# Optimization experiments

Measured on AMD Instinct MI355X. Metric: run time of the kernel, lower is better.

The kernel has to match this reference:

```python
import jax, jax.numpy as jnp
import numpy as np

N, IN_CH, HID, OUT = 3072, 128, 256, 32
HEADS = 12


def setup_inputs() -> dict:
    key = jax.random.key(0)
    ks = jax.random.split(key, 16)

    def glorot(k, shape):
        fan_in, fan_out = shape[0], shape[-1]
        lim = float(np.sqrt(6.0 / (fan_in + fan_out)))
        return jax.random.uniform(k, shape, jnp.float32, -lim, lim)

    return {
        "x": jax.random.normal(ks[0], (N, IN_CH), jnp.float32),
        "attn_tensor": jax.random.normal(ks[1], (HEADS, N, N), jnp.float32),
        "edge_weight": jnp.ones((1,), jnp.float32),  # unused (use_edge_weight=False)
        "batch_idx": jnp.zeros((N,), jnp.int64),      # single graph
        # Conv2d(12,1,1) == per-head scalar mix
        "agg_w": jax.random.normal(ks[2], (HEADS,), jnp.float32) * 0.1,
        "agg_b": jnp.zeros((1,), jnp.float32),
        # GCNConv weights (x @ W then propagate, + bias)
        "W1": glorot(ks[3], (IN_CH, HID)), "b1": jnp.zeros((HID,), jnp.float32),
        "W2": glorot(ks[4], (HID, HID)),   "b2": jnp.zeros((HID,), jnp.float32),
        # final MLP: Linear -> ReLU -> LayerNorm -> Linear
        "lin1_W": glorot(ks[5], (HID, HID)), "lin1_b": jnp.zeros((HID,), jnp.float32),
        "ln_g": jnp.ones((HID,), jnp.float32), "ln_b": jnp.zeros((HID,), jnp.float32),
        "lin2_W": glorot(ks[6], (HID, OUT)), "lin2_b": jnp.zeros((OUT,), jnp.float32),
    }


def reference(x, attn_tensor, edge_weight, batch_idx,
              agg_w, agg_b, W1, b1, W2, b2,
              lin1_W, lin1_b, ln_g, ln_b, lin2_W, lin2_b):
    threshold = 0.0
    n = x.shape[0]

    # Conv2d(12,1,kernel_size=1): weighted sum over heads -> [N, N] score matrix
    agg = jnp.einsum('c,cij->ij', agg_w, attn_tensor) + agg_b[0]

    # thresholded adjacency (mask.nonzero() -> edge_index), kept dense in jax
    A = (agg > threshold).astype(x.dtype)  # A[s, t] = edge s->t

    # PyG gcn_norm with add_remaining_self_loops (binary weights -> diag = 1)
    eye = jnp.eye(n, dtype=x.dtype)
    A_hat = A * (1.0 - eye) + eye
    deg = A_hat.sum(axis=0)                        # in-degree at target nodes
    dinv = jnp.where(deg > 0, jax.lax.rsqrt(deg), 0.0)
    A_norm = dinv[:, None] * A_hat * dinv[None, :]  # norm = dinv[src] * dinv[dst]

    # GCNConv 1: out[t] = sum_s A_norm[s,t] (x W)[s] + b
    h = jnp.einsum('st,sd->td', A_norm, x @ W1) + b1
    h = jax.nn.relu(h)
    # GCNConv 2
    h = jnp.einsum('st,sd->td', A_norm, h @ W2) + b2

    # global_mean_pool over batch_idx (single graph here)
    bi = batch_idx.astype(jnp.int32)
    sums = jax.ops.segment_sum(h, bi, num_segments=1)
    counts = jax.ops.segment_sum(jnp.ones((n,), h.dtype), bi, num_segments=1)
    g = sums / counts[:, None]

    # Linear -> ReLU -> LayerNorm -> Linear
    z = jax.nn.relu(g @ lin1_W + lin1_b)
    mu = z.mean(axis=-1, keepdims=True)
    var = ((z - mu) ** 2).mean(axis=-1, keepdims=True)
    z = (z - mu) * jax.lax.rsqrt(var + 1e-5) * ln_g + ln_b
    out = z @ lin2_W + lin2_b
    return out
```

## Files before the change

kernel.cpp:

```cpp
#include <hip/hip_runtime.h>
#include <hip/hip_bf16.h>

#define NN     3072
#define NW32   96
#define INCH   128
#define HID    256
#define NHEADS 12
#define PLANE  9437184LL

typedef __attribute__((ext_vector_type(8))) short     s16x8;
typedef __attribute__((ext_vector_type(4))) float     f32x4;
typedef __attribute__((ext_vector_type(8))) unsigned short u16x8;
typedef __attribute__((ext_vector_type(4))) unsigned int   u32x4;

__device__ inline unsigned short bf16_rne(float f) {
    unsigned int u = __float_as_uint(f);
    u += 0x7FFFu + ((u >> 16) & 1u);
    return (unsigned short)(u >> 16);
}

__global__ __launch_bounds__(256) void k_adj_y1(const float* __restrict__ attn,
                                                const float* __restrict__ agg_w,
                                                const float* __restrict__ agg_b,
                                                const float* __restrict__ x,
                                                const float* __restrict__ W1,
                                                unsigned int* __restrict__ maskT32,
                                                unsigned short* __restrict__ y1t) {
    __shared__ unsigned int chunkU[4][64];
    __shared__ float xs[8][INCH];

    if (blockIdx.x < 1152) {
        const int w = threadIdx.x >> 6, l = threadIdx.x & 63;
        const int t0 = (blockIdx.x % 12) * 256;
        const int s0 = (blockIdx.x / 12) * 32;
        const int tb = t0 + 4 * l;

        float wc[NHEADS];
#pragma unroll
        for (int c = 0; c < NHEADS; ++c) wc[c] = agg_w[c];
        const float bias = agg_b[0];

        const float* base = attn + (long long)(s0 + 8 * w) * NN + tb;
        unsigned int colb = 0;
#pragma unroll 2
        for (int i = 0; i < 8; ++i) {
            const int s = s0 + 8 * w + i;
            const float* ps = base + (long long)i * NN;
            f32x4 acc = {bias, bias, bias, bias};
#pragma unroll
            for (int c = 0; c < NHEADS; ++c) {
                f32x4 v = *(const f32x4*)(ps + c * PLANE);
                acc[0] = fmaf(wc[c], v[0], acc[0]);
                acc[1] = fmaf(wc[c], v[1], acc[1]);
                acc[2] = fmaf(wc[c], v[2], acc[2]);
                acc[3] = fmaf(wc[c], v[3], acc[3]);
            }
            unsigned int bset = 0;
            bset |= (acc[0] > 0.0f || s == tb + 0) ? (1u << i)        : 0u;
            bset |= (acc[1] > 0.0f || s == tb + 1) ? (1u << (8 + i))  : 0u;
            bset |= (acc[2] > 0.0f || s == tb + 2) ? (1u << (16 + i)) : 0u;
            bset |= (acc[3] > 0.0f || s == tb + 3) ? (1u << (24 + i)) : 0u;
            colb |= bset;
        }
        chunkU[w][l] = colb;
        __syncthreads();
        const int l2 = threadIdx.x >> 2, j = threadIdx.x & 3;
        unsigned int word =  ((chunkU[0][l2] >> (8 * j)) & 0xFFu)
                          | (((chunkU[1][l2] >> (8 * j)) & 0xFFu) << 8)
                          | (((chunkU[2][l2] >> (8 * j)) & 0xFFu) << 16)
                          | (((chunkU[3][l2] >> (8 * j)) & 0xFFu) << 24);
        maskT32[(long long)(t0 + threadIdx.x) * NW32 + (s0 >> 5)] = word;
    } else {
        int s0 = (blockIdx.x - 1152) * 8;
        for (int i = threadIdx.x; i < 8 * INCH; i += 256)
            xs[i >> 7][i & 127] = x[s0 * INCH + i];
        __syncthreads();
        int d = threadIdx.x;
        float acc[8] = {0, 0, 0, 0, 0, 0, 0, 0};
        for (int k = 0; k < INCH; ++k) {
            float w = W1[k * HID + d];
#pragma unroll
            for (int r = 0; r < 8; ++r) acc[r] = fmaf(xs[r][k], w, acc[r]);
        }
        u16x8 v;
#pragma unroll
        for (int r = 0; r < 8; ++r) v[r] = bf16_rne(acc[r]);
        *(u16x8*)(y1t + (long long)d * NN + s0) = v;
    }
}

__global__ __launch_bounds__(256) void k_dinv(const unsigned int* __restrict__ maskT32,
                                              float* __restrict__ dinv,
                                              unsigned short* __restrict__ dinvb) {
    int t = blockIdx.x * 256 + threadIdx.x;
    const u32x4* row = (const u32x4*)(maskT32 + (long long)t * NW32);
    int deg = 0;
#pragma unroll
    for (int i = 0; i < 24; ++i) {
        u32x4 v = row[i];
        deg += __popc(v[0]) + __popc(v[1]) + __popc(v[2]) + __popc(v[3]);
    }
    float di = rsqrtf((float)deg);
    dinv[t] = di;
    dinvb[t] = bf16_rne(di);
}

__global__ __launch_bounds__(256) void k_prop(const unsigned int* __restrict__ maskT32,
                                              const unsigned short* __restrict__ dinvb,
                                              const unsigned short* __restrict__ y1t,
                                              const float* __restrict__ dinv,
                                              float* __restrict__ partials,
                                              float* __restrict__ w2p) {
    if (blockIdx.x < 384) {
        const int w = threadIdx.x >> 6, l = threadIdx.x & 63;
        const int lr = l & 15, lg = l >> 4;
        const int t0 = (blockIdx.x % 48) * 64 + w * 16;
        const int d0 = ((blockIdx.x / 48) % 2) * 128;
        const int z  = blockIdx.x / 96;

        const unsigned long long* mrow =
            (const unsigned long long*)(maskT32 + (long long)(t0 + lr) * NW32) + z * 12;

        const unsigned short* B[8];
#pragma unroll
        for (int n = 0; n < 8; ++n)
            B[n] = y1t + (long long)(d0 + n * 16 + lr) * NN;

        f32x4 acc[8];
#pragma unroll
        for (int n = 0; n < 8; ++n) acc[n] = (f32x4){0.f, 0.f, 0.f, 0.f};

#pragma unroll 2
        for (int kw = 0; kw < 12; ++kw) {
            unsigned long long word = mrow[kw];
#pragma unroll
            for (int half = 0; half < 2; ++half) {
                const int k0 = z * 768 + kw * 64 + half * 32 + lg * 8;
                unsigned int bits = (unsigned int)((word >> (half * 32 + lg * 8)) & 0xFFULL);
                u16x8 dv = *(const u16x8*)(dinvb + k0);
                s16x8 av;
#pragma unroll
                for (int j = 0; j < 8; ++j)
                    av[j] = ((bits >> j) & 1u) ? (short)dv[j] : (short)0;
#pragma unroll
                for (int n = 0; n < 8; ++n) {
                    s16x8 bv = *(const s16x8*)(const void*)(B[n] + k0);
                    acc[n] = __builtin_amdgcn_mfma_f32_16x16x32_bf16(av, bv, acc[n], 0, 0, 0);
                }
            }
        }

        const int trow = t0 + lg * 4;
#pragma unroll
        for (int n = 0; n < 8; ++n) {
            const int d = d0 + n * 16 + lr;
#pragma unroll
            for (int r = 0; r < 4; ++r)
                partials[((size_t)z * NN + trow + r) * HID + d] = acc[n][r];
        }
    } else {
        __shared__ float red[4][64];
        const int r = blockIdx.x - 384;
        const int wq = r % 48;
        const int tc = r / 48;
        const int wv = threadIdx.x >> 6, l = threadIdx.x & 63;
        const unsigned long long* mt = (const unsigned long long*)maskT32;
        float acc = 0.0f;
#pragma unroll 4
        for (int it = 0; it < 64; ++it) {
            const int t = tc * 256 + wv * 64 + it;
            unsigned long long word = mt[(long long)t * 48 + wq];
            acc += ((word >> l) & 1ULL) ? dinv[t] : 0.0f;
        }
        red[wv][l] = acc;
        __syncthreads();
        if (threadIdx.x < 64)
            w2p[tc * NN + wq * 64 + threadIdx.x] =
                red[0][threadIdx.x] + red[1][threadIdx.x] + red[2][threadIdx.x] + red[3][threadIdx.x];
    }
}

__global__ __launch_bounds__(256) void k_vred(const float* __restrict__ partials,
                                              const float* __restrict__ dinv,
                                              const float* __restrict__ b1,
                                              const float* __restrict__ w2p,
                                              float* __restrict__ vp) {
    __shared__ float w2s[8];
    const int b = blockIdx.x, d = threadIdx.x;
    if (threadIdx.x < 8) {
        const int t = b * 8 + threadIdx.x;
        float a = 0.0f;
#pragma unroll
        for (int tc = 0; tc < 12; ++tc) a += w2p[tc * NN + t];
        w2s[threadIdx.x] = dinv[t] * a;
    }
    __syncthreads();
    const float bb = b1[d];
    float vacc = 0.0f;
#pragma unroll
    for (int i = 0; i < 8; ++i) {
        const int t = b * 8 + i;
        float ssum = partials[((size_t)0 * NN + t) * HID + d]
                   + partials[((size_t)1 * NN + t) * HID + d]
                   + partials[((size_t)2 * NN + t) * HID + d]
                   + partials[((size_t)3 * NN + t) * HID + d];
        float h = fmaxf(fmaf(dinv[t], ssum, bb), 0.0f);
        vacc = fmaf(w2s[i], h, vacc);
    }
    vp[b * HID + d] = vacc;
}

__global__ __launch_bounds__(256) void k_head(const float* __restrict__ vp,
                                              const float* __restrict__ W2,
                                              const float* __restrict__ b2,
                                              const float* __restrict__ l1W,
                                              const float* __restrict__ l1b,
                                              const float* __restrict__ lng,
                                              const float* __restrict__ lnb,
                                              const float* __restrict__ l2W,
                                              const float* __restrict__ l2b,
                                              float* __restrict__ out) {
    __shared__ float vs[HID], gs[HID], zs[HID], red[4];
    int d = threadIdx.x;
    float v = 0.0f;
    for (int c = 0; c < 384; ++c) v += vp[c * HID + d];
    vs[d] = v;
    __syncthreads();
    float a = 0.0f;
    for (int k = 0; k < HID; ++k) a = fmaf(vs[k], W2[k * HID + d], a);
    gs[d] = b2[d] + a * (1.0f / 3072.0f);
    __syncthreads();
    float z1 = l1b[d];
    for (int k = 0; k < HID; ++k) z1 = fmaf(gs[k], l1W[k * HID + d], z1);
    z1 = fmaxf(z1, 0.0f);
    float sum = z1;
    for (int o = 1; o < 64; o <<= 1) sum += __shfl_xor(sum, o);
    if ((d & 63) == 0) red[d >> 6] = sum;
    __syncthreads();
    float mu = (red[0] + red[1] + red[2] + red[3]) * (1.0f / 256.0f);
    __syncthreads();
    float diff = z1 - mu, sq = diff * diff;
    for (int o = 1; o < 64; o <<= 1) sq += __shfl_xor(sq, o);
    if ((d & 63) == 0) red[d >> 6] = sq;
    __syncthreads();
    float var = (red[0] + red[1] + red[2] + red[3]) * (1.0f / 256.0f);
    float zn = diff * rsqrtf(var + 1e-5f) * lng[d] + lnb[d];
    zs[d] = zn;
    __syncthreads();
    if (d < 32) {
        float o = l2b[d];
        for (int k = 0; k < HID; ++k) o = fmaf(zs[k], l2W[k * 32 + d], o);
        out[d] = o;
    }
}

extern "C" void kernel_launch(void* const* d_in, const int* in_sizes, int n_in,
                              void* d_out, int out_size, void* d_ws, size_t ws_size,
                              hipStream_t stream) {
    const float* x     = (const float*)d_in[0];
    const float* attn  = (const float*)d_in[1];
    const float* agg_w = (const float*)d_in[4];
    const float* agg_b = (const float*)d_in[5];
    const float* W1    = (const float*)d_in[6];
    const float* b1    = (const float*)d_in[7];
    const float* W2    = (const float*)d_in[8];
    const float* b2    = (const float*)d_in[9];
    const float* l1W   = (const float*)d_in[10];
    const float* l1b   = (const float*)d_in[11];
    const float* lng   = (const float*)d_in[12];
    const float* lnb   = (const float*)d_in[13];
    const float* l2W   = (const float*)d_in[14];
    const float* l2b   = (const float*)d_in[15];
    float* out = (float*)d_out;

    char* ws = (char*)d_ws;
    size_t off = 0;
    auto alloc = [&](size_t bytes) -> void* {
        off = (off + 255) & ~(size_t)255;
        void* p = ws + off;
        off += bytes;
        return p;
    };
    unsigned int*   maskT32 = (unsigned int*)alloc((size_t)NN * NW32 * 4);
    float*          dinv  = (float*)alloc((size_t)NN * 4);
    unsigned short* dinvb = (unsigned short*)alloc((size_t)NN * 2);
    float*          w2p   = (float*)alloc((size_t)12 * NN * 4);
    unsigned short* y1t   = (unsigned short*)alloc((size_t)HID * NN * 2);
    float*          part  = (float*)alloc((size_t)4 * NN * HID * 4);
    float*          vp    = (float*)alloc((size_t)384 * HID * 4);

    hipLaunchKernelGGL(k_adj_y1, dim3(1536), dim3(256), 0, stream,
                       attn, agg_w, agg_b, x, W1, maskT32, y1t);
    hipLaunchKernelGGL(k_dinv,   dim3(12),   dim3(256), 0, stream, maskT32, dinv, dinvb);
    hipLaunchKernelGGL(k_prop,   dim3(960),  dim3(256), 0, stream,
                       maskT32, dinvb, y1t, dinv, part, w2p);
    hipLaunchKernelGGL(k_vred,   dim3(384),  dim3(256), 0, stream, part, dinv, b1, w2p, vp);
    hipLaunchKernelGGL(k_head,   dim3(1),    dim3(256), 0, stream,
                       vp, W2, b2, l1W, l1b, lng, lnb, l2W, l2b, out);
}
```

Baseline: 191.7 us.

## Reorder head-mix loads with nontemporal hints and fuse final head via last-block counter

The adjacency kernel now loops over heads outermost, keeping eight row accumulators in registers and issuing nontemporal loads over the large attention tensor. The bias becomes a negated threshold in the comparison. The separate single-block head kernel is folded into the reduction kernel: a global atomic counter, reset in the degree kernel, lets the last finishing block run the MLP head, removing one launch. This adds threadfence and atomic overhead and more register pressure in the adjacency kernel.

```diff
diff --git a/kernel.cpp b/kernel.cpp
--- a/kernel.cpp
+++ b/kernel.cpp
@@ -34,33 +34,36 @@
         const int t0 = (blockIdx.x % 12) * 256;
         const int s0 = (blockIdx.x / 12) * 32;
         const int tb = t0 + 4 * l;
-
-        float wc[NHEADS];
-#pragma unroll
-        for (int c = 0; c < NHEADS; ++c) wc[c] = agg_w[c];
-        const float bias = agg_b[0];
-
-        const float* base = attn + (long long)(s0 + 8 * w) * NN + tb;
+        const int srow = s0 + 8 * w;
+        const float thr = -agg_b[0];
+
+        f32x4 acc[8];
+#pragma unroll
+        for (int i = 0; i < 8; ++i) acc[i] = (f32x4){0.f, 0.f, 0.f, 0.f};
+
+        const int voff = srow * NN + tb;
+#pragma unroll 1
+        for (int c = 0; c < NHEADS; ++c) {
+            const float* pc = attn + (long long)c * PLANE;
+            const float wcv = agg_w[c];
+#pragma unroll
+            for (int i = 0; i < 8; ++i) {
+                f32x4 v = __builtin_nontemporal_load((const f32x4*)(pc + voff + i * NN));
+                acc[i][0] = fmaf(wcv, v[0], acc[i][0]);
+                acc[i][1] = fmaf(wcv, v[1], acc[i][1]);
+                acc[i][2] = fmaf(wcv, v[2], acc[i][2]);
+                acc[i][3] = fmaf(wcv, v[3], acc[i][3]);
+            }
+        }
+
         unsigned int colb = 0;
-#pragma unroll 2
+#pragma unroll
         for (int i = 0; i < 8; ++i) {
-            const int s = s0 + 8 * w + i;
-            const float* ps = base + (long long)i * NN;
-            f32x4 acc = {bias, bias, bias, bias};
-#pragma unroll
-            for (int c = 0; c < NHEADS; ++c) {
-                f32x4 v = *(const f32x4*)(ps + c * PLANE);
-                acc[0] = fmaf(wc[c], v[0], acc[0]);
-                acc[1] = fmaf(wc[c], v[1], acc[1]);
-                acc[2] = fmaf(wc[c], v[2], acc[2]);
-                acc[3] = fmaf(wc[c], v[3], acc[3]);
-            }
-            unsigned int bset = 0;
-            bset |= (acc[0] > 0.0f || s == tb + 0) ? (1u << i)        : 0u;
-            bset |= (acc[1] > 0.0f || s == tb + 1) ? (1u << (8 + i))  : 0u;
-            bset |= (acc[2] > 0.0f || s == tb + 2) ? (1u << (16 + i)) : 0u;
-            bset |= (acc[3] > 0.0f || s == tb + 3) ? (1u << (24 + i)) : 0u;
-            colb |= bset;
+            const int s = srow + i;
+            colb |= ((acc[i][0] > thr || s == tb + 0) ? 1u : 0u) << (0 + i);
+            colb |= ((acc[i][1] > thr || s == tb + 1) ? 1u : 0u) << (8 + i);
+            colb |= ((acc[i][2] > thr || s == tb + 2) ? 1u : 0u) << (16 + i);
+            colb |= ((acc[i][3] > thr || s == tb + 3) ? 1u : 0u) << (24 + i);
         }
         chunkU[w][l] = colb;
         __syncthreads();
@@ -91,7 +94,9 @@
 
 __global__ __launch_bounds__(256) void k_dinv(const unsigned int* __restrict__ maskT32,
                                               float* __restrict__ dinv,
-                                              unsigned short* __restrict__ dinvb) {
+                                              unsigned short* __restrict__ dinvb,
+                                              unsigned int* __restrict__ cnt) {
+    if (blockIdx.x == 0 && threadIdx.x == 0) *cnt = 0u;
     int t = blockIdx.x * 256 + threadIdx.x;
     const u32x4* row = (const u32x4*)(maskT32 + (long long)t * NW32);
     int deg = 0;
@@ -180,12 +185,23 @@
     }
 }
 
-__global__ __launch_bounds__(256) void k_vred(const float* __restrict__ partials,
-                                              const float* __restrict__ dinv,
-                                              const float* __restrict__ b1,
-                                              const float* __restrict__ w2p,
-                                              float* __restrict__ vp) {
+__global__ __launch_bounds__(256) void k_vredhead(const float* __restrict__ partials,
+                                                  const float* __restrict__ dinv,
+                                                  const float* __restrict__ b1,
+                                                  const float* __restrict__ w2p,
+                                                  float* __restrict__ vp,
+                                                  unsigned int* __restrict__ cnt,
+                                                  const float* __restrict__ W2,
+                                                  const float* __restrict__ b2,
+                                                  const float* __restrict__ l1W,
+                                                  const float* __restrict__ l1b,
+                                                  const float* __restrict__ lng,
+                                                  const float* __restrict__ lnb,
+                                                  const float* __restrict__ l2W,
+                                                  const float* __restrict__ l2b,
+                                                  float* __restrict__ out) {
     __shared__ float w2s[8];
+    __shared__ int islast;
     const int b = blockIdx.x, d = threadIdx.x;
     if (threadIdx.x < 8) {
         const int t = b * 8 + threadIdx.x;
@@ -208,20 +224,14 @@
         vacc = fmaf(w2s[i], h, vacc);
     }
     vp[b * HID + d] = vacc;
-}
-
-__global__ __launch_bounds__(256) void k_head(const float* __restrict__ vp,
-                                              const float* __restrict__ W2,
-                                              const float* __restrict__ b2,
-                                              const float* __restrict__ l1W,
-                                              const float* __restrict__ l1b,
-                                              const float* __restrict__ lng,
-                                              const float* __restrict__ lnb,
-                                              const float* __restrict__ l2W,
-                                              const float* __restrict__ l2b,
-                                              float* __restrict__ out) {
+    __threadfence();
+    if (threadIdx.x == 0)
+        islast = (atomicAdd(cnt, 1u) == 383u) ? 1 : 0;
+    __syncthreads();
+    if (!islast) return;
+    __threadfence();
+
     __shared__ float vs[HID], gs[HID], zs[HID], red[4];
-    int d = threadIdx.x;
     float v = 0.0f;
     for (int c = 0; c < 384; ++c) v += vp[c * HID + d];
     vs[d] = v;
@@ -288,13 +298,14 @@
     unsigned short* y1t   = (unsigned short*)alloc((size_t)HID * NN * 2);
     float*          part  = (float*)alloc((size_t)4 * NN * HID * 4);
     float*          vp    = (float*)alloc((size_t)384 * HID * 4);
-
-    hipLaunchKernelGGL(k_adj_y1, dim3(1536), dim3(256), 0, stream,
+    unsigned int*   cnt   = (unsigned int*)alloc(4);
+
+    hipLaunchKernelGGL(k_adj_y1,   dim3(1536), dim3(256), 0, stream,
                        attn, agg_w, agg_b, x, W1, maskT32, y1t);
-    hipLaunchKernelGGL(k_dinv,   dim3(12),   dim3(256), 0, stream, maskT32, dinv, dinvb);
-    hipLaunchKernelGGL(k_prop,   dim3(960),  dim3(256), 0, stream,
+    hipLaunchKernelGGL(k_dinv,     dim3(12),   dim3(256), 0, stream, maskT32, dinv, dinvb, cnt);
+    hipLaunchKernelGGL(k_prop,     dim3(960),  dim3(256), 0, stream,
                        maskT32, dinvb, y1t, dinv, part, w2p);
-    hipLaunchKernelGGL(k_vred,   dim3(384),  dim3(256), 0, stream, part, dinv, b1, w2p, vp);
-    hipLaunchKernelGGL(k_head,   dim3(1),    dim3(256), 0, stream,
-                       vp, W2, b2, l1W, l1b, lng, lnb, l2W, l2b, out);
-}
+    hipLaunchKernelGGL(k_vredhead, dim3(384),  dim3(256), 0, stream,
+                       part, dinv, b1, w2p, vp, cnt,
+                       W2, b2, l1W, l1b, lng, lnb, l2W, l2b, out);
+}
```

New measurement: 194.9 us. No clear change (+1.7%).
